# Performance work log

Measured on AMD Instinct MI355X. Metric: run time of the kernel, lower is better.

The kernel has to match this reference:

```python
import jax, jax.numpy as jnp
import numpy as np

NEG_INF = -9e15  # matches torch's -9000000000000000.0 mask value


def setup_inputs() -> dict:
    key = jax.random.key(0)
    k1, k2, k3, k4 = jax.random.split(key, 4)
    B, F_in, T, N, F_out = 8, 64, 12, 512, 64
    inp = {
        "input": jax.random.normal(k1, (B, F_in, T, N), dtype=jnp.float32),
        "adj": jax.random.randint(k2, (B, T, N, N), 0, 2, dtype=jnp.int32),
        "W": jax.random.normal(k3, (F_in, F_out), dtype=jnp.float32),
        "a": jax.random.normal(k4, (2 * F_out, 1), dtype=jnp.float32),
    }
    return inp


def reference(input, adj, W, a):
    # input: [B, F_in, T, N], adj: [B, T, N, N]
    F_out = W.shape[1]
    x = jnp.transpose(input, (0, 2, 3, 1))          # [B, T, N, F_in]
    Wh = jnp.einsum('btnf,fo->btno', x, W)          # [B, T, N, F_out]
    # score decomposition: e[i,j] = leakyrelu(a1.Wh_i + a2.Wh_j)
    a1 = a[:F_out, 0]
    a2 = a[F_out:, 0]
    f1 = Wh @ a1                                    # [B, T, N]
    f2 = Wh @ a2                                    # [B, T, N]
    e = jax.nn.leaky_relu(f1[..., :, None] + f2[..., None, :], 0.2)
    e = jnp.where(adj > 0, e, NEG_INF)
    attn = jax.nn.softmax(e, axis=-1)               # [B, T, N, N]
    h = jnp.einsum('btij,btjo->btio', attn, Wh)     # [B, T, N, F_out]
    return jax.nn.elu(h)                            # concat=True -> elu
```

## Files before the change

kernel.cpp:

```cpp
#include <hip/hip_runtime.h>
#include <hip/hip_bf16.h>

typedef float fx4 __attribute__((ext_vector_type(4)));
typedef short i16x8 __attribute__((ext_vector_type(8)));
typedef unsigned short u16;

#define NEG_INF_F (-9.0e15f)

__device__ inline u16 f2bf(float v){
  __hip_bfloat16 h = __float2bfloat16(v);
  return *reinterpret_cast<u16*>(&h);
}

__global__ __launch_bounds__(256) void gat_compress(
    const int* __restrict__ adj, unsigned* __restrict__ maskw)
{
  const int t = blockIdx.x * 256 + threadIdx.x;
  const uint4* src = (const uint4*)adj + (size_t)t * 8;
  uint4 v[8];
  #pragma unroll
  for (int i = 0; i < 8; ++i) v[i] = src[i];
  unsigned m = 0u;
  #pragma unroll
  for (int i = 0; i < 8; ++i) {
    if ((int)v[i].x > 0) m |= 1u << (4*i+0);
    if ((int)v[i].y > 0) m |= 1u << (4*i+1);
    if ((int)v[i].z > 0) m |= 1u << (4*i+2);
    if ((int)v[i].w > 0) m |= 1u << (4*i+3);
  }
  maskw[t] = m;
}

__global__ __launch_bounds__(256) void gat_prep(
    const float* __restrict__ input,
    const float* __restrict__ W,
    const float* __restrict__ Avec,
    u16*   __restrict__ whB,
    float* __restrict__ f1w,
    float* __restrict__ f2w)
{
  __shared__ float Wl[64*64];
  __shared__ float Al[128];
  __shared__ u16   Rp[16384];
  const int tid = threadIdx.x;
  const int bt  = blockIdx.y;
  const int b   = bt / 12, t = bt % 12;
  const int xb  = blockIdx.x;
  const int n   = xb * 256 + tid;

  {
    const fx4* src = (const fx4*)W;
    fx4* dst = (fx4*)Wl;
    #pragma unroll
    for (int i = 0; i < 4; ++i) dst[tid + 256*i] = src[tid + 256*i];
    if (tid < 32) ((fx4*)Al)[tid] = ((const fx4*)Avec)[tid];
  }
  __syncthreads();

  const float* xp = input + ((size_t)b*64*12 + t) * 512 + n;

  fx4 acc[16];
  #pragma unroll
  for (int i = 0; i < 16; ++i) acc[i] = (fx4){0.f,0.f,0.f,0.f};

  #pragma unroll 8
  for (int f = 0; f < 64; ++f) {
    float xv = xp[(size_t)f * 6144];
    const fx4* wr = (const fx4*)(Wl + f*64);
    #pragma unroll
    for (int o4 = 0; o4 < 16; ++o4) acc[o4] += xv * wr[o4];
  }

  float s1 = 0.f, s2 = 0.f;
  #pragma unroll
  for (int o4 = 0; o4 < 16; ++o4) {
    fx4 v  = acc[o4];
    fx4 w1 = ((const fx4*)Al)[o4];
    fx4 w2 = ((const fx4*)Al)[o4 + 16];
    s1 += v[0]*w1[0] + v[1]*w1[1] + v[2]*w1[2] + v[3]*w1[3];
    s2 += v[0]*w2[0] + v[1]*w2[1] + v[2]*w2[2] + v[3]*w2[3];
  }
  f1w[bt*512 + n] = s1;
  f2w[bt*512 + n] = s2;

  const int ktl  = (n >> 5) & 7;
  const int q    = (n >> 3) & 3;
  const int e    = n & 7;
  const int rowb = ktl*2048 + q*128 + e;
  #pragma unroll
  for (int o4 = 0; o4 < 16; ++o4) {
    #pragma unroll
    for (int c = 0; c < 4; ++c) {
      const int o = o4*4 + c;
      Rp[rowb + (o >> 4)*512 + (o & 15)*8] = f2bf(acc[o4][c]);
    }
  }
  __syncthreads();

  uint4* dst = (uint4*)(whB + ((size_t)bt*16 + xb*8) * 2048);
  const uint4* src = (const uint4*)Rp;
  #pragma unroll
  for (int i = 0; i < 8; ++i) dst[tid + 256*i] = src[tid + 256*i];
}

__global__ __launch_bounds__(256, 4) void gat_attn(
    const unsigned* __restrict__ maskw,
    const u16*   __restrict__ whB,
    const float* __restrict__ f1w,
    const float* __restrict__ f2w,
    float*       __restrict__ out)
{
  __shared__ float f2l[512];
  __shared__ float f1l[16];
  __shared__ float wmaxl[4];
  __shared__ float sums[16];
  __shared__ unsigned maskl[16][16];
  __shared__ u16   attnl[16*512];

  const int tid = threadIdx.x;
  const int l   = tid & 63;
  const int w   = tid >> 6;
  const int bt  = blockIdx.y;
  const int it  = blockIdx.x;

  ((unsigned*)maskl)[tid] = maskw[((size_t)bt*512 + it*16)*16 + tid];
  float2 fv = ((const float2*)(f2w + bt*512))[tid];
  ((float2*)f2l)[tid] = fv;
  float m2 = fmaxf(fv.x, fv.y);
  #pragma unroll
  for (int off = 32; off >= 1; off >>= 1) m2 = fmaxf(m2, __shfl_xor(m2, off));
  if (l == 0) wmaxl[w] = m2;
  if (tid < 16) f1l[tid] = f1w[bt*512 + it*16 + tid];
  __syncthreads();
  const float F2max = fmaxf(fmaxf(wmaxl[0], wmaxl[1]), fmaxf(wmaxl[2], wmaxl[3]));

  const fx4 f20 = ((const fx4*)f2l)[l];
  const fx4 f21 = ((const fx4*)f2l)[64 + l];
  fx4 v0, v1, vh0, vh1;
  #pragma unroll
  for (int c = 0; c < 4; ++c) {
    v0[c]  = __expf(f20[c] - F2max);
    v1[c]  = __expf(f21[c] - F2max);
    vh0[c] = __expf(0.2f*(f20[c] - F2max));
    vh1[c] = __expf(0.2f*(f21[c] - F2max));
  }

  const int R0 = w * 4;
  const int wi = l >> 3;
  const int sh = (l & 7) * 4;

  float ssum[4];
  #pragma unroll
  for (int r = 0; r < 4; ++r) {
    const int rowR = R0 + r;
    const unsigned nib0 = (maskl[rowR][wi]     >> sh) & 0xFu;
    const unsigned nib1 = (maskl[rowR][8 + wi] >> sh) & 0xFu;
    const float f1v = f1l[rowR];

    float mx = NEG_INF_F;
    mx = fmaxf(mx, (nib0 & 1u) ? f20[0] : NEG_INF_F);
    mx = fmaxf(mx, (nib0 & 2u) ? f20[1] : NEG_INF_F);
    mx = fmaxf(mx, (nib0 & 4u) ? f20[2] : NEG_INF_F);
    mx = fmaxf(mx, (nib0 & 8u) ? f20[3] : NEG_INF_F);
    mx = fmaxf(mx, (nib1 & 1u) ? f21[0] : NEG_INF_F);
    mx = fmaxf(mx, (nib1 & 2u) ? f21[1] : NEG_INF_F);
    mx = fmaxf(mx, (nib1 & 4u) ? f21[2] : NEG_INF_F);
    mx = fmaxf(mx, (nib1 & 8u) ? f21[3] : NEG_INF_F);
    #pragma unroll
    for (int off = 32; off >= 1; off >>= 1) mx = fmaxf(mx, __shfl_xor(mx, off));

    const float tM = f1v + mx;
    const float M  = fmaxf(tM, 0.2f*tM);
    const float gap = F2max - mx;

    float sum = 0.f;
    ushort4 pk0, pk1;
    if (gap <= 80.f) {
      const float u  = __expf(f1v + F2max - M);
      const float uh = __expf(0.2f*(f1v + F2max) - M);
      const float thr = -f1v;
      float pv;
#define GAT_F(pkf, bb_, ff, vv, vvh) { \
      const bool cpos = (ff) > thr; \
      float a = cpos ? (vv) : (vvh); \
      float bb = cpos ? u : uh; \
      pv = (bb_) ? a*bb : 0.f; sum += pv; pkf = f2bf(pv); }
      GAT_F(pk0.x, nib0 & 1u, f20[0], v0[0], vh0[0])
      GAT_F(pk0.y, nib0 & 2u, f20[1], v0[1], vh0[1])
      GAT_F(pk0.z, nib0 & 4u, f20[2], v0[2], vh0[2])
      GAT_F(pk0.w, nib0 & 8u, f20[3], v0[3], vh0[3])
      GAT_F(pk1.x, nib1 & 1u, f21[0], v1[0], vh1[0])
      GAT_F(pk1.y, nib1 & 2u, f21[1], v1[1], vh1[1])
      GAT_F(pk1.z, nib1 & 4u, f21[2], v1[2], vh1[2])
      GAT_F(pk1.w, nib1 & 8u, f21[3], v1[3], vh1[3])
#undef GAT_F
    } else {
      const float Mf = (mx == NEG_INF_F) ? NEG_INF_F : M;
      float pv;
#define GAT_S(pkf, bb_, ff) { float s = f1v + (ff); float lr = fmaxf(s, 0.2f*s); \
      float ee = (bb_) ? lr : NEG_INF_F; \
      pv = __expf(ee - Mf); sum += pv; pkf = f2bf(pv); }
      GAT_S(pk0.x, nib0 & 1u, f20[0]) GAT_S(pk0.y, nib0 & 2u, f20[1])
      GAT_S(pk0.z, nib0 & 4u, f20[2]) GAT_S(pk0.w, nib0 & 8u, f20[3])
      GAT_S(pk1.x, nib1 & 1u, f21[0]) GAT_S(pk1.y, nib1 & 2u, f21[1])
      GAT_S(pk1.z, nib1 & 4u, f21[2]) GAT_S(pk1.w, nib1 & 8u, f21[3])
#undef GAT_S
    }
    ssum[r] = sum;

    const unsigned swz = (unsigned)((rowR & 7) << 4);
    char* base = (char*)attnl + rowR * 1024;
    *(ushort4*)(base + (((unsigned)(      8*l)) ^ swz)) = pk0;
    *(ushort4*)(base + (((unsigned)(512 + 8*l)) ^ swz)) = pk1;
  }

  #pragma unroll
  for (int r = 0; r < 4; ++r) {
    #pragma unroll
    for (int off = 32; off >= 1; off >>= 1) ssum[r] += __shfl_xor(ssum[r], off);
  }
  if (l == 0) {
    #pragma unroll
    for (int r = 0; r < 4; ++r) sums[R0 + r] = ssum[r];
  }
  __syncthreads();

  const int r = l & 15, q = l >> 4;
  const int ct = w;
  const unsigned swzB = (unsigned)((r & 7) << 4);
  const char* aBase = (const char*)attnl + r * 1024;
  const u16*  wp    = whB + (size_t)bt*32768 + ct*512 + l*8;
  fx4 acc = {0,0,0,0};

  #pragma unroll
  for (int kt = 0; kt < 16; ++kt) {
    i16x8 af = *(const i16x8*)(aBase + (((unsigned)(kt*64 + q*16)) ^ swzB));
    i16x8 bf = *(const i16x8*)(wp + kt*2048);
    acc = __builtin_amdgcn_mfma_f32_16x16x32_bf16(af, bf, acc, 0, 0, 0);
  }

  float* op = out + ((size_t)bt*512 + it*16) * 64;
  #pragma unroll
  for (int rr = 0; rr < 4; ++rr) {
    const float rs = 1.0f / sums[q*4 + rr];
    float v = acc[rr] * rs;
    v = v > 0.f ? v : expm1f(v);
    op[(q*4 + rr)*64 + ct*16 + r] = v;
  }
}

extern "C" void kernel_launch(void* const* d_in, const int* in_sizes, int n_in,
                              void* d_out, int out_size, void* d_ws, size_t ws_size,
                              hipStream_t stream) {
  const float* input = (const float*)d_in[0];
  const int*   adj   = (const int*)  d_in[1];
  const float* W     = (const float*)d_in[2];
  const float* Avec  = (const float*)d_in[3];
  float* out = (float*)d_out;

  char* ws = (char*)d_ws;
  u16*      whB   = (u16*)ws;
  float*    f1w   = (float*)(ws + 6291456);
  float*    f2w   = (float*)(ws + 6291456 + 196608);
  unsigned* maskw = (unsigned*)(ws + 6291456 + 393216);

  gat_compress<<<3072, 256, 0, stream>>>(adj, maskw);
  gat_prep<<<dim3(2, 96), 256, 0, stream>>>(input, W, Avec, whB, f1w, f2w);
  gat_attn<<<dim3(32, 96), 256, 0, stream>>>(maskw, whB, f1w, f2w, out);
}
```

Before: 56.54 us.

## Merge compress and prep kernels, simplify softmax probability path, compute row sums via MFMA

Merges the adjacency-compress and projection kernels into one launch, with block ranges picking the role, which saves one kernel launch and lets the two run concurrently. In the attention kernel the per-row masked max reduction is replaced with a global-max fast path, taken when any unmasked entry lies near the global f2 max. That path uses a max-of-two-products form and a LUT bitmask to zero masked bf16 pairs. Row sums are now taken from an extra MFMA against a ones vector in wave 0 instead of shuffle reductions, which costs an extra barrier. The fast path gives up some numerical headroom in exchange for fewer instructions.

```diff
diff --git a/kernel.cpp b/kernel.cpp
--- a/kernel.cpp
+++ b/kernel.cpp
@@ -11,42 +11,47 @@
   __hip_bfloat16 h = __float2bfloat16(v);
   return *reinterpret_cast<u16*>(&h);
 }
-
-__global__ __launch_bounds__(256) void gat_compress(
-    const int* __restrict__ adj, unsigned* __restrict__ maskw)
-{
-  const int t = blockIdx.x * 256 + threadIdx.x;
-  const uint4* src = (const uint4*)adj + (size_t)t * 8;
-  uint4 v[8];
-  #pragma unroll
-  for (int i = 0; i < 8; ++i) v[i] = src[i];
-  unsigned m = 0u;
-  #pragma unroll
-  for (int i = 0; i < 8; ++i) {
-    if ((int)v[i].x > 0) m |= 1u << (4*i+0);
-    if ((int)v[i].y > 0) m |= 1u << (4*i+1);
-    if ((int)v[i].z > 0) m |= 1u << (4*i+2);
-    if ((int)v[i].w > 0) m |= 1u << (4*i+3);
-  }
-  maskw[t] = m;
-}
-
-__global__ __launch_bounds__(256) void gat_prep(
+__device__ inline unsigned pk2(float lo, float hi){
+  return (unsigned)f2bf(lo) | ((unsigned)f2bf(hi) << 16);
+}
+
+__global__ __launch_bounds__(256) void gat_pre(
     const float* __restrict__ input,
     const float* __restrict__ W,
     const float* __restrict__ Avec,
-    u16*   __restrict__ whB,
-    float* __restrict__ f1w,
-    float* __restrict__ f2w)
+    const int*   __restrict__ adj,
+    u16*      __restrict__ whB,
+    float*    __restrict__ f1w,
+    float*    __restrict__ f2w,
+    unsigned* __restrict__ maskw)
 {
   __shared__ float Wl[64*64];
   __shared__ float Al[128];
   __shared__ u16   Rp[16384];
+  const int bid = blockIdx.x;
   const int tid = threadIdx.x;
-  const int bt  = blockIdx.y;
-  const int b   = bt / 12, t = bt % 12;
-  const int xb  = blockIdx.x;
-  const int n   = xb * 256 + tid;
+
+  if (bid >= 192) {
+    const int t = (bid - 192) * 256 + tid;
+    const uint4* src = (const uint4*)adj + (size_t)t * 8;
+    uint4 v[8];
+    #pragma unroll
+    for (int i = 0; i < 8; ++i) v[i] = src[i];
+    unsigned m = 0u;
+    #pragma unroll
+    for (int i = 0; i < 8; ++i) {
+      if ((int)v[i].x > 0) m |= 1u << (4*i+0);
+      if ((int)v[i].y > 0) m |= 1u << (4*i+1);
+      if ((int)v[i].z > 0) m |= 1u << (4*i+2);
+      if ((int)v[i].w > 0) m |= 1u << (4*i+3);
+    }
+    maskw[t] = m;
+    return;
+  }
+
+  const int bt = bid >> 1, xb = bid & 1;
+  const int b  = bt / 12, t = bt % 12;
+  const int n  = xb * 256 + tid;
 
   {
     const fx4* src = (const fx4*)W;
@@ -110,11 +115,11 @@
     const float* __restrict__ f2w,
     float*       __restrict__ out)
 {
-  __shared__ float f2l[512];
   __shared__ float f1l[16];
   __shared__ float wmaxl[4];
   __shared__ float sums[16];
   __shared__ unsigned maskl[16][16];
+  __shared__ uint2 lutl[16];
   __shared__ u16   attnl[16*512];
 
   const int tid = threadIdx.x;
@@ -124,18 +129,23 @@
   const int it  = blockIdx.x;
 
   ((unsigned*)maskl)[tid] = maskw[((size_t)bt*512 + it*16)*16 + tid];
-  float2 fv = ((const float2*)(f2w + bt*512))[tid];
-  ((float2*)f2l)[tid] = fv;
-  float m2 = fmaxf(fv.x, fv.y);
+  if (tid < 16) f1l[tid] = f1w[bt*512 + it*16 + tid];
+  if (tid < 16) {
+    const unsigned nb = tid;
+    lutl[tid] = (uint2){ ((nb&1u)?0xFFFFu:0u) | ((nb&2u)?0xFFFF0000u:0u),
+                         ((nb&4u)?0xFFFFu:0u) | ((nb&8u)?0xFFFF0000u:0u) };
+  }
+  const float* f2p = f2w + bt*512;
+  const fx4 f20 = ((const fx4*)f2p)[l];
+  const fx4 f21 = ((const fx4*)f2p)[64 + l];
+  float m2 = fmaxf(fmaxf(fmaxf(f20[0], f20[1]), fmaxf(f20[2], f20[3])),
+                   fmaxf(fmaxf(f21[0], f21[1]), fmaxf(f21[2], f21[3])));
   #pragma unroll
   for (int off = 32; off >= 1; off >>= 1) m2 = fmaxf(m2, __shfl_xor(m2, off));
   if (l == 0) wmaxl[w] = m2;
-  if (tid < 16) f1l[tid] = f1w[bt*512 + it*16 + tid];
   __syncthreads();
   const float F2max = fmaxf(fmaxf(wmaxl[0], wmaxl[1]), fmaxf(wmaxl[2], wmaxl[3]));
 
-  const fx4 f20 = ((const fx4*)f2l)[l];
-  const fx4 f21 = ((const fx4*)f2l)[64 + l];
   fx4 v0, v1, vh0, vh1;
   #pragma unroll
   for (int c = 0; c < 4; ++c) {
@@ -144,12 +154,16 @@
     vh0[c] = __expf(0.2f*(f20[c] - F2max));
     vh1[c] = __expf(0.2f*(f21[c] - F2max));
   }
+  const float thrBig = F2max - 80.f;
+  const unsigned big_lo = (f20[0] > thrBig ? 1u : 0u) | (f20[1] > thrBig ? 2u : 0u)
+                        | (f20[2] > thrBig ? 4u : 0u) | (f20[3] > thrBig ? 8u : 0u);
+  const unsigned big_hi = (f21[0] > thrBig ? 1u : 0u) | (f21[1] > thrBig ? 2u : 0u)
+                        | (f21[2] > thrBig ? 4u : 0u) | (f21[3] > thrBig ? 8u : 0u);
 
   const int R0 = w * 4;
   const int wi = l >> 3;
   const int sh = (l & 7) * 4;
 
-  float ssum[4];
   #pragma unroll
   for (int r = 0; r < 4; ++r) {
     const int rowR = R0 + r;
@@ -157,87 +171,81 @@
     const unsigned nib1 = (maskl[rowR][8 + wi] >> sh) & 0xFu;
     const float f1v = f1l[rowR];
 
-    float mx = NEG_INF_F;
-    mx = fmaxf(mx, (nib0 & 1u) ? f20[0] : NEG_INF_F);
-    mx = fmaxf(mx, (nib0 & 2u) ? f20[1] : NEG_INF_F);
-    mx = fmaxf(mx, (nib0 & 4u) ? f20[2] : NEG_INF_F);
-    mx = fmaxf(mx, (nib0 & 8u) ? f20[3] : NEG_INF_F);
-    mx = fmaxf(mx, (nib1 & 1u) ? f21[0] : NEG_INF_F);
-    mx = fmaxf(mx, (nib1 & 2u) ? f21[1] : NEG_INF_F);
-    mx = fmaxf(mx, (nib1 & 4u) ? f21[2] : NEG_INF_F);
-    mx = fmaxf(mx, (nib1 & 8u) ? f21[3] : NEG_INF_F);
-    #pragma unroll
-    for (int off = 32; off >= 1; off >>= 1) mx = fmaxf(mx, __shfl_xor(mx, off));
-
-    const float tM = f1v + mx;
-    const float M  = fmaxf(tM, 0.2f*tM);
-    const float gap = F2max - mx;
-
-    float sum = 0.f;
-    ushort4 pk0, pk1;
-    if (gap <= 80.f) {
-      const float u  = __expf(f1v + F2max - M);
-      const float uh = __expf(0.2f*(f1v + F2max) - M);
-      const float thr = -f1v;
-      float pv;
-#define GAT_F(pkf, bb_, ff, vv, vvh) { \
-      const bool cpos = (ff) > thr; \
-      float a = cpos ? (vv) : (vvh); \
-      float bb = cpos ? u : uh; \
-      pv = (bb_) ? a*bb : 0.f; sum += pv; pkf = f2bf(pv); }
-      GAT_F(pk0.x, nib0 & 1u, f20[0], v0[0], vh0[0])
-      GAT_F(pk0.y, nib0 & 2u, f20[1], v0[1], vh0[1])
-      GAT_F(pk0.z, nib0 & 4u, f20[2], v0[2], vh0[2])
-      GAT_F(pk0.w, nib0 & 8u, f20[3], v0[3], vh0[3])
-      GAT_F(pk1.x, nib1 & 1u, f21[0], v1[0], vh1[0])
-      GAT_F(pk1.y, nib1 & 2u, f21[1], v1[1], vh1[1])
-      GAT_F(pk1.z, nib1 & 4u, f21[2], v1[2], vh1[2])
-      GAT_F(pk1.w, nib1 & 8u, f21[3], v1[3], vh1[3])
-#undef GAT_F
+    unsigned w0, w1, w2, w3;
+    const unsigned sb = (nib0 & big_lo) | (nib1 & big_hi);
+    if (__builtin_expect(__any((int)sb), 1)) {
+      const float tR = f1v + F2max;
+      const float M  = fmaxf(tR, 0.2f*tR);
+      const float u  = __expf(tR - M);
+      const float uh = __expf(0.2f*tR - M);
+      fx4 PA, PB;
+      #pragma unroll
+      for (int c = 0; c < 4; ++c) {
+        PA[c] = fmaxf(u*v0[c], uh*vh0[c]);
+        PB[c] = fmaxf(u*v1[c], uh*vh1[c]);
+      }
+      const uint2 mA = lutl[nib0];
+      const uint2 mB = lutl[nib1];
+      w0 = pk2(PA[0], PA[1]) & mA.x;
+      w1 = pk2(PA[2], PA[3]) & mA.y;
+      w2 = pk2(PB[0], PB[1]) & mB.x;
+      w3 = pk2(PB[2], PB[3]) & mB.y;
     } else {
-      const float Mf = (mx == NEG_INF_F) ? NEG_INF_F : M;
-      float pv;
-#define GAT_S(pkf, bb_, ff) { float s = f1v + (ff); float lr = fmaxf(s, 0.2f*s); \
-      float ee = (bb_) ? lr : NEG_INF_F; \
-      pv = __expf(ee - Mf); sum += pv; pkf = f2bf(pv); }
-      GAT_S(pk0.x, nib0 & 1u, f20[0]) GAT_S(pk0.y, nib0 & 2u, f20[1])
-      GAT_S(pk0.z, nib0 & 4u, f20[2]) GAT_S(pk0.w, nib0 & 8u, f20[3])
-      GAT_S(pk1.x, nib1 & 1u, f21[0]) GAT_S(pk1.y, nib1 & 2u, f21[1])
-      GAT_S(pk1.z, nib1 & 4u, f21[2]) GAT_S(pk1.w, nib1 & 8u, f21[3])
+      float mx = NEG_INF_F;
+      mx = fmaxf(mx, (nib0 & 1u) ? f20[0] : NEG_INF_F);
+      mx = fmaxf(mx, (nib0 & 2u) ? f20[1] : NEG_INF_F);
+      mx = fmaxf(mx, (nib0 & 4u) ? f20[2] : NEG_INF_F);
+      mx = fmaxf(mx, (nib0 & 8u) ? f20[3] : NEG_INF_F);
+      mx = fmaxf(mx, (nib1 & 1u) ? f21[0] : NEG_INF_F);
+      mx = fmaxf(mx, (nib1 & 2u) ? f21[1] : NEG_INF_F);
+      mx = fmaxf(mx, (nib1 & 4u) ? f21[2] : NEG_INF_F);
+      mx = fmaxf(mx, (nib1 & 8u) ? f21[3] : NEG_INF_F);
+      #pragma unroll
+      for (int off = 32; off >= 1; off >>= 1) mx = fmaxf(mx, __shfl_xor(mx, off));
+      const float tM = f1v + mx;
+      const float Mc = fmaxf(tM, 0.2f*tM);
+      const float Mf = (mx == NEG_INF_F) ? NEG_INF_F : Mc;
+      float pv[8];
+#define GAT_S(idx, bb_, ff) { float s = f1v + (ff); float lr = fmaxf(s, 0.2f*s); \
+      float ee = (bb_) ? lr : NEG_INF_F; pv[idx] = __expf(ee - Mf); }
+      GAT_S(0, nib0 & 1u, f20[0]) GAT_S(1, nib0 & 2u, f20[1])
+      GAT_S(2, nib0 & 4u, f20[2]) GAT_S(3, nib0 & 8u, f20[3])
+      GAT_S(4, nib1 & 1u, f21[0]) GAT_S(5, nib1 & 2u, f21[1])
+      GAT_S(6, nib1 & 4u, f21[2]) GAT_S(7, nib1 & 8u, f21[3])
 #undef GAT_S
+      w0 = pk2(pv[0], pv[1]); w1 = pk2(pv[2], pv[3]);
+      w2 = pk2(pv[4], pv[5]); w3 = pk2(pv[6], pv[7]);
     }
-    ssum[r] = sum;
 
     const unsigned swz = (unsigned)((rowR & 7) << 4);
     char* base = (char*)attnl + rowR * 1024;
-    *(ushort4*)(base + (((unsigned)(      8*l)) ^ swz)) = pk0;
-    *(ushort4*)(base + (((unsigned)(512 + 8*l)) ^ swz)) = pk1;
-  }
-
-  #pragma unroll
-  for (int r = 0; r < 4; ++r) {
-    #pragma unroll
-    for (int off = 32; off >= 1; off >>= 1) ssum[r] += __shfl_xor(ssum[r], off);
-  }
-  if (l == 0) {
-    #pragma unroll
-    for (int r = 0; r < 4; ++r) sums[R0 + r] = ssum[r];
+    *(uint2*)(base + (((unsigned)(      8*l)) ^ swz)) = (uint2){w0, w1};
+    *(uint2*)(base + (((unsigned)(512 + 8*l)) ^ swz)) = (uint2){w2, w3};
   }
   __syncthreads();
 
   const int r = l & 15, q = l >> 4;
-  const int ct = w;
   const unsigned swzB = (unsigned)((r & 7) << 4);
   const char* aBase = (const char*)attnl + r * 1024;
-  const u16*  wp    = whB + (size_t)bt*32768 + ct*512 + l*8;
-  fx4 acc = {0,0,0,0};
+  const u16*  wp    = whB + (size_t)bt*32768 + w*512 + l*8;
+  i16x8 bones;
+  #pragma unroll
+  for (int e = 0; e < 8; ++e) bones[e] = (short)0x3F80;
+  fx4 acc = {0,0,0,0}, accS = {0,0,0,0};
 
   #pragma unroll
   for (int kt = 0; kt < 16; ++kt) {
     i16x8 af = *(const i16x8*)(aBase + (((unsigned)(kt*64 + q*16)) ^ swzB));
     i16x8 bf = *(const i16x8*)(wp + kt*2048);
     acc = __builtin_amdgcn_mfma_f32_16x16x32_bf16(af, bf, acc, 0, 0, 0);
-  }
+    if (w == 0)
+      accS = __builtin_amdgcn_mfma_f32_16x16x32_bf16(af, bones, accS, 0, 0, 0);
+  }
+  if (w == 0 && r == 0) {
+    #pragma unroll
+    for (int rr = 0; rr < 4; ++rr) sums[q*4 + rr] = accS[rr];
+  }
+  __syncthreads();
 
   float* op = out + ((size_t)bt*512 + it*16) * 64;
   #pragma unroll
@@ -245,7 +253,7 @@
     const float rs = 1.0f / sums[q*4 + rr];
     float v = acc[rr] * rs;
     v = v > 0.f ? v : expm1f(v);
-    op[(q*4 + rr)*64 + ct*16 + r] = v;
+    op[(q*4 + rr)*64 + w*16 + r] = v;
   }
 }
 
@@ -264,7 +272,7 @@
   float*    f2w   = (float*)(ws + 6291456 + 196608);
   unsigned* maskw = (unsigned*)(ws + 6291456 + 393216);
 
-  gat_compress<<<3072, 256, 0, stream>>>(adj, maskw);
-  gat_prep<<<dim3(2, 96), 256, 0, stream>>>(input, W, Avec, whB, f1w, f2w);
+  gat_pre<<<192 + 3072, 256, 0, stream>>>(input, W, Avec, adj,
+                                          whB, f1w, f2w, maskw);
   gat_attn<<<dim3(32, 96), 256, 0, stream>>>(maskw, whB, f1w, f2w, out);
 }
```

New measurement: 51.35 us. 9.2% less time.
